# Kernel tuning notes

Measured on AMD Instinct MI355X. Metric: run time of the kernel, lower is better.

Reference implementation:

```python
import jax, jax.numpy as jnp
import numpy as np

NUM_NODES = 100000
NUM_EDGES = 50000
N_INC = 1000000  # incidence pairs (node, hyperedge)
IN_DIM = 128
EDGE_DIM = 128
NODE_DIM = 128


def _glorot(key, fan_in, fan_out):
    lim = float(np.sqrt(6.0 / (fan_in + fan_out)))
    return jax.random.uniform(key, (fan_in, fan_out), jnp.float32, -lim, lim)


def _prelu(x, a):
    return jnp.where(x >= 0, x, a * x)


def setup_inputs() -> dict:
    key = jax.random.key(0)
    ks = jax.random.split(key, 7)
    x = jax.random.normal(ks[0], (NUM_NODES, IN_DIM), jnp.float32)
    node_idx = jax.random.randint(ks[1], (N_INC,), 0, NUM_NODES, jnp.int32)
    edge_idx = jax.random.randint(ks[2], (N_INC,), 0, NUM_EDGES, jnp.int32)
    hyperedge_index = jnp.stack([node_idx, edge_idx])  # [2, N_INC]
    return dict(
        x=x,
        hyperedge_index=hyperedge_index,
        W_n2e_0=_glorot(ks[3], IN_DIM, EDGE_DIM),
        W_e2n_0=_glorot(ks[4], EDGE_DIM, NODE_DIM),
        bias_0=jnp.zeros((NODE_DIM,), jnp.float32),
        W_n2e_1=_glorot(ks[5], NODE_DIM, EDGE_DIM),
        W_e2n_1=_glorot(ks[6], EDGE_DIM, NODE_DIM),
        bias_1=jnp.zeros((NODE_DIM,), jnp.float32),
        alpha=jnp.float32(0.25),  # shared nn.PReLU() parameter
        num_nodes=NUM_NODES,
        num_edges=NUM_EDGES,
    )


def _conv(x, node_idx, edge_idx, Dn_inv, De_inv, W_n2e, W_e2n, b, alpha,
          num_nodes, num_edges):
    # node -> hyperedge: row-normalized scatter-add (norm = De^{-1} per target edge)
    xe = x @ W_n2e                                              # [N, E_dim]
    msg_e = xe[node_idx] * De_inv[edge_idx][:, None]            # [N_INC, E_dim]
    e = jax.ops.segment_sum(msg_e, edge_idx, num_segments=num_edges)
    e = _prelu(e, alpha)
    # hyperedge -> node: norm = Dn^{-1} per target node
    xn = e @ W_e2n                                              # [M, D]
    msg_n = xn[edge_idx] * Dn_inv[node_idx][:, None]            # [N_INC, D]
    n = jax.ops.segment_sum(msg_n, node_idx, num_segments=num_nodes) + b
    return n, e


def reference(x, hyperedge_index, W_n2e_0, W_e2n_0, bias_0, W_n2e_1, W_e2n_1,
              bias_1, alpha, num_nodes, num_edges):
    node_idx = hyperedge_index[0]
    edge_idx = hyperedge_index[1]
    ones = jnp.ones((node_idx.shape[0],), jnp.float32)
    Dn = jax.ops.segment_sum(ones, node_idx, num_segments=num_nodes)
    De = jax.ops.segment_sum(ones, edge_idx, num_segments=num_edges)
    Dn_inv = jnp.where(Dn > 0, 1.0 / jnp.where(Dn > 0, Dn, 1.0), 0.0)
    De_inv = jnp.where(De > 0, 1.0 / jnp.where(De > 0, De, 1.0), 0.0)

    n, e = _conv(x, node_idx, edge_idx, Dn_inv, De_inv,
                 W_n2e_0, W_e2n_0, bias_0, alpha, num_nodes, num_edges)
    n = _prelu(n, alpha)  # encoder-level activation between layers
    n, e = _conv(n, node_idx, edge_idx, Dn_inv, De_inv,
                 W_n2e_1, W_e2n_1, bias_1, alpha, num_nodes, num_edges)
    n = _prelu(n, alpha)
    return n, e
```

## Files before the change

### kernel.cpp

```cpp
#include <hip/hip_runtime.h>
#include <stdint.h>

#define NN 100000
#define NE 50000
#define NBLK 256
#define NBK 196
#define ESH 8
#define NSH 9

using bf16x8 = __attribute__((ext_vector_type(8))) short;
using f32x4  = __attribute__((ext_vector_type(4))) float;

__device__ inline unsigned f2bf(float f) {
  union { float f; unsigned u; } x; x.f = f;
  unsigned u = x.u;
  return (u + 0x7FFFu + ((u >> 16) & 1u)) >> 16;
}
__device__ inline float bfbits2f(unsigned bits) {
  union { unsigned u; float f; } x; x.u = bits;
  return x.f;
}


__global__ __launch_bounds__(256) void hist_kernel(const int* __restrict__ nidx,
                                                   const int* __restrict__ eidx, int ni,
                                                   int* __restrict__ He, int* __restrict__ Hn) {
  __shared__ int he[NBK], hn[NBK];
  for (int t = threadIdx.x; t < NBK; t += 256) { he[t] = 0; hn[t] = 0; }
  __syncthreads();
  int chunk = (ni + NBLK - 1) / NBLK;
  int s = blockIdx.x * chunk, e = min(s + chunk, ni);
  for (int i = s + threadIdx.x; i < e; i += 256) {
    atomicAdd(&he[eidx[i] >> ESH], 1);
    atomicAdd(&hn[nidx[i] >> NSH], 1);
  }
  __syncthreads();
  for (int t = threadIdx.x; t < NBK; t += 256) {
    He[t * NBLK + blockIdx.x] = he[t];
    Hn[t * NBLK + blockIdx.x] = hn[t];
  }
}

__global__ __launch_bounds__(256) void scanH_kernel(int* __restrict__ He, int* __restrict__ Hn,
                                                    int* __restrict__ ebb, int* __restrict__ nbb,
                                                    int ni) {
  int* H = blockIdx.x ? Hn : He;
  int* bb = blockIdx.x ? nbb : ebb;
  __shared__ int tot[256];
  int t = threadIdx.x;
  int sum = 0;
  if (t < NBK)
    for (int b = 0; b < NBLK; b++) sum += H[t * NBLK + b];
  tot[t] = sum;
  __syncthreads();
  for (int o = 1; o < 256; o <<= 1) {
    int v = (t >= o) ? tot[t - o] : 0;
    __syncthreads();
    tot[t] += v;
    __syncthreads();
  }
  int base = (t > 0) ? tot[t - 1] : 0;
  if (t < NBK) {
    bb[t] = base;
    int run = base;
    for (int b = 0; b < NBLK; b++) {
      int old = H[t * NBLK + b];
      H[t * NBLK + b] = run;
      run += old;
    }
  }
  if (t == 0) bb[NBK] = ni;
}

__global__ __launch_bounds__(256) void scatter_kernel(const int* __restrict__ nidx,
                                                      const int* __restrict__ eidx, int ni,
                                                      const int* __restrict__ He,
                                                      const int* __restrict__ Hn,
                                                      int2* __restrict__ binE,
                                                      int2* __restrict__ binN) {
  __shared__ int ce[NBK], cn[NBK];
  for (int t = threadIdx.x; t < NBK; t += 256) {
    ce[t] = He[t * NBLK + blockIdx.x];
    cn[t] = Hn[t * NBLK + blockIdx.x];
  }
  __syncthreads();
  int chunk = (ni + NBLK - 1) / NBLK;
  int s = blockIdx.x * chunk, e = min(s + chunk, ni);
  for (int i = s + threadIdx.x; i < e; i += 256) {
    int nd = nidx[i], ed = eidx[i];
    int pe = atomicAdd(&ce[ed >> ESH], 1);
    binE[pe] = make_int2(nd, ed);
    int pn = atomicAdd(&cn[nd >> NSH], 1);
    binN[pn] = make_int2(ed, nd);
  }
}

__global__ __launch_bounds__(256) void finalize_kernel(const int2* __restrict__ binE,
                                                       const int2* __restrict__ binN,
                                                       const int* __restrict__ ebb,
                                                       const int* __restrict__ nbb,
                                                       int* __restrict__ eoff, int* __restrict__ noff,
                                                       float* __restrict__ einv, float* __restrict__ ninv,
                                                       int* __restrict__ edge_nodes,
                                                       int* __restrict__ node_edges, int ni) {
  __shared__ int cnt[512], excl[512], sc[256];
  bool isE = blockIdx.x < NBK;
  int b = isE ? blockIdx.x : blockIdx.x - NBK;
  const int2* bin = isE ? binE : binN;
  const int* bb = isE ? ebb : nbb;
  int* off = isE ? eoff : noff;
  float* inv = isE ? einv : ninv;
  int* out = isE ? edge_nodes : node_edges;
  int NT = isE ? NE : NN;
  int sh = isE ? ESH : NSH;
  int tbase = b << sh;
  int nt = min(1 << sh, NT - tbase);
  int t = threadIdx.x;
  cnt[t] = 0; cnt[t + 256] = 0;
  __syncthreads();
  int s = bb[b], e = bb[b + 1];
  for (int i = s + t; i < e; i += 256) atomicAdd(&cnt[bin[i].y - tbase], 1);
  __syncthreads();
  int p = cnt[2 * t] + cnt[2 * t + 1];
  sc[t] = p;
  __syncthreads();
  for (int o = 1; o < 256; o <<= 1) {
    int v = (t >= o) ? sc[t - o] : 0;
    __syncthreads();
    sc[t] += v;
    __syncthreads();
  }
  int pb = (t > 0) ? sc[t - 1] : 0;
  excl[2 * t] = pb;
  excl[2 * t + 1] = pb + cnt[2 * t];
  __syncthreads();
  for (int lt = t; lt < nt; lt += 256) {
    off[tbase + lt] = s + excl[lt];
    int c = cnt[lt];
    inv[tbase + lt] = (c > 0) ? 1.0f / (float)c : 0.0f;
  }
  if (b == NBK - 1 && t == 0) off[NT] = ni;
  __syncthreads();
  cnt[t] = 0; cnt[t + 256] = 0;
  __syncthreads();
  for (int i = s + t; i < e; i += 256) {
    int2 it = bin[i];
    int lt = it.y - tbase;
    int pos = s + excl[lt] + atomicAdd(&cnt[lt], 1);
    out[pos] = it.x;
  }
}

__global__ void packw_kernel(const float* __restrict__ w0, const float* __restrict__ w1,
                             const float* __restrict__ w2, const float* __restrict__ w3,
                             short* __restrict__ wp) {
  int gid = blockIdx.x * blockDim.x + threadIdx.x;
  if (gid >= 4 * 16384) return;
  int w = gid >> 14, r = gid & 16383;
  int j = r & 7, lane = (r >> 3) & 63, kk = (r >> 9) & 3, ct = (r >> 11) & 7;
  int k = kk * 32 + (lane >> 4) * 8 + j;
  int c = ct * 16 + (lane & 15);
  const float* W = (w == 0) ? w0 : (w == 1) ? w1 : (w == 2) ? w2 : w3;
  wp[gid] = (short)f2bf(W[k * 128 + c]);
}

template <bool ABF>
__global__ __launch_bounds__(256) void gemm_kernel(const void* __restrict__ Ap,
                                                   const short* __restrict__ Wp,
                                                   short* __restrict__ C, int M) {
  int wave = threadIdx.x >> 6;
  int lane = threadIdx.x & 63;
  int rt = blockIdx.x * 4 + wave;
  if (rt * 16 >= M) return;
  int kg = lane >> 4;
  int rloc = lane & 15;
  bf16x8 a[4];
  if constexpr (ABF) {
    const short* arow = (const short*)Ap + (size_t)(rt * 16 + rloc) * 128 + kg * 8;
#pragma unroll
    for (int kk = 0; kk < 4; kk++) a[kk] = *(const bf16x8*)(arow + kk * 32);
  } else {
    const float* arow = (const float*)Ap + (size_t)(rt * 16 + rloc) * 128 + kg * 8;
#pragma unroll
    for (int kk = 0; kk < 4; kk++) {
      float4 lo = *(const float4*)(arow + kk * 32);
      float4 hi = *(const float4*)(arow + kk * 32 + 4);
      bf16x8 tv;
      tv[0] = (short)f2bf(lo.x); tv[1] = (short)f2bf(lo.y);
      tv[2] = (short)f2bf(lo.z); tv[3] = (short)f2bf(lo.w);
      tv[4] = (short)f2bf(hi.x); tv[5] = (short)f2bf(hi.y);
      tv[6] = (short)f2bf(hi.z); tv[7] = (short)f2bf(hi.w);
      a[kk] = tv;
    }
  }
#pragma unroll
  for (int ct = 0; ct < 8; ct++) {
    f32x4 acc = {0.f, 0.f, 0.f, 0.f};
#pragma unroll
    for (int kk = 0; kk < 4; kk++) {
      bf16x8 bfr = *(const bf16x8*)(Wp + ((size_t)(ct * 4 + kk) * 64 + lane) * 8);
      acc = __builtin_amdgcn_mfma_f32_16x16x32_bf16(a[kk], bfr, acc, 0, 0, 0);
    }
    size_t cbase = (size_t)(rt * 16 + kg * 4) * 128 + ct * 16 + rloc;
#pragma unroll
    for (int j = 0; j < 4; j++) C[cbase + (size_t)j * 128] = (short)f2bf(acc[j]);
  }
}

template <bool OBF>
__global__ __launch_bounds__(256) void gather_kernel(const uint4* __restrict__ src,
                                                     void* __restrict__ dst,
                                                     const int* __restrict__ off,
                                                     const int* __restrict__ ids,
                                                     const float* __restrict__ inv,
                                                     const float* __restrict__ bias,
                                                     const float* __restrict__ alpha_p, int T) {
  int tgt = blockIdx.x * 16 + (threadIdx.x >> 4);
  if (tgt >= T) return;
  int c = threadIdx.x & 15;
  int s = off[tgt], e = off[tgt + 1];
  float a0 = 0, a1 = 0, a2 = 0, a3 = 0, a4 = 0, a5 = 0, a6 = 0, a7 = 0;
  for (int i = s; i < e; i++) {
    int sid = ids[i];
    uint4 v = src[(size_t)sid * 16 + c];
    a0 += bfbits2f(v.x << 16); a1 += bfbits2f(v.x & 0xffff0000u);
    a2 += bfbits2f(v.y << 16); a3 += bfbits2f(v.y & 0xffff0000u);
    a4 += bfbits2f(v.z << 16); a5 += bfbits2f(v.z & 0xffff0000u);
    a6 += bfbits2f(v.w << 16); a7 += bfbits2f(v.w & 0xffff0000u);
  }
  float scv = inv[tgt];
  float al = *alpha_p;
  float b[8] = {0, 0, 0, 0, 0, 0, 0, 0};
  if (bias) {
    float4 b0 = ((const float4*)bias)[c * 2];
    float4 b1 = ((const float4*)bias)[c * 2 + 1];
    b[0] = b0.x; b[1] = b0.y; b[2] = b0.z; b[3] = b0.w;
    b[4] = b1.x; b[5] = b1.y; b[6] = b1.z; b[7] = b1.w;
  }
  float r[8] = {a0, a1, a2, a3, a4, a5, a6, a7};
#pragma unroll
  for (int j = 0; j < 8; j++) {
    float v = r[j] * scv + b[j];
    r[j] = (v >= 0.f) ? v : al * v;
  }
  if constexpr (OBF) {
    uint4 o;
    o.x = (f2bf(r[0]) & 0xffffu) | (f2bf(r[1]) << 16);
    o.y = (f2bf(r[2]) & 0xffffu) | (f2bf(r[3]) << 16);
    o.z = (f2bf(r[4]) & 0xffffu) | (f2bf(r[5]) << 16);
    o.w = (f2bf(r[6]) & 0xffffu) | (f2bf(r[7]) << 16);
    ((uint4*)dst)[(size_t)tgt * 16 + c] = o;
  } else {
    float4 o0; o0.x = r[0]; o0.y = r[1]; o0.z = r[2]; o0.w = r[3];
    float4 o1; o1.x = r[4]; o1.y = r[5]; o1.z = r[6]; o1.w = r[7];
    ((float4*)dst)[(size_t)tgt * 32 + c * 2] = o0;
    ((float4*)dst)[(size_t)tgt * 32 + c * 2 + 1] = o1;
  }
}

extern "C" void kernel_launch(void* const* d_in, const int* in_sizes, int n_in,
                              void* d_out, int out_size, void* d_ws, size_t ws_size,
                              hipStream_t stream) {
  const float* x = (const float*)d_in[0];
  const int* nidx = (const int*)d_in[1];
  int NI = in_sizes[1] / 2;
  const int* eidx = nidx + NI;
  const float* W0 = (const float*)d_in[2];
  const float* W1 = (const float*)d_in[3];
  const float* b0 = (const float*)d_in[4];
  const float* W2 = (const float*)d_in[5];
  const float* W3 = (const float*)d_in[6];
  const float* b1 = (const float*)d_in[7];
  const float* alpha = (const float*)d_in[8];

  char* ws = (char*)d_ws;
  size_t o = 0;
  auto alloc = [&](size_t bytes) { void* p = ws + o; o += (bytes + 255) & ~255ull; return p; };
  int* He = (int*)alloc((size_t)NBK * NBLK * 4);
  int* Hn = (int*)alloc((size_t)NBK * NBLK * 4);
  int* ebb = (int*)alloc((NBK + 1) * 4);
  int* nbb = (int*)alloc((NBK + 1) * 4);
  int* eoff = (int*)alloc((size_t)(NE + 1) * 4);
  int* noff = (int*)alloc((size_t)(NN + 1) * 4);
  float* einv = (float*)alloc((size_t)NE * 4);
  float* ninv = (float*)alloc((size_t)NN * 4);
  int* edge_nodes = (int*)alloc((size_t)NI * 4);
  int* node_edges = (int*)alloc((size_t)NI * 4);
  short* wp = (short*)alloc((size_t)4 * 16384 * 2);
  char* arena = (char*)alloc((size_t)NN * 128 * 2 * 2 + (size_t)NE * 128 * 2 * 2);
  int2* binE = (int2*)arena;
  int2* binN = (int2*)(arena + (size_t)NI * 8);
  short* bufNb = (short*)arena;
  short* bufEb = (short*)(arena + (size_t)NN * 128 * 2);
  short* n0b = (short*)(arena + (size_t)NN * 128 * 2 + (size_t)NE * 128 * 2);
  short* e0b = (short*)(arena + (size_t)NN * 128 * 4 + (size_t)NE * 128 * 2);

  float* outN = (float*)d_out;
  float* outE = outN + (size_t)NN * 128;

  hist_kernel<<<NBLK, 256, 0, stream>>>(nidx, eidx, NI, He, Hn);
  scanH_kernel<<<2, 256, 0, stream>>>(He, Hn, ebb, nbb, NI);
  scatter_kernel<<<NBLK, 256, 0, stream>>>(nidx, eidx, NI, He, Hn, binE, binN);
  finalize_kernel<<<2 * NBK, 256, 0, stream>>>(binE, binN, ebb, nbb, eoff, noff,
                                               einv, ninv, edge_nodes, node_edges, NI);
  packw_kernel<<<256, 256, 0, stream>>>(W0, W1, W2, W3, wp);

  int gN = (NN / 16 + 3) / 4, gE = (NE / 16 + 3) / 4;
  gemm_kernel<false><<<gN, 256, 0, stream>>>(x, wp + 0 * 16384, bufNb, NN);
  gather_kernel<true><<<(NE + 15) / 16, 256, 0, stream>>>((const uint4*)bufNb, e0b,
                                                          eoff, edge_nodes, einv, nullptr, alpha, NE);
  gemm_kernel<true><<<gE, 256, 0, stream>>>(e0b, wp + 1 * 16384, bufEb, NE);
  gather_kernel<true><<<(NN + 15) / 16, 256, 0, stream>>>((const uint4*)bufEb, n0b,
                                                          noff, node_edges, ninv, b0, alpha, NN);
  gemm_kernel<true><<<gN, 256, 0, stream>>>(n0b, wp + 2 * 16384, bufNb, NN);
  gather_kernel<false><<<(NE + 15) / 16, 256, 0, stream>>>((const uint4*)bufNb, outE,
                                                           eoff, edge_nodes, einv, nullptr, alpha, NE);
  gemm_kernel<false><<<gE, 256, 0, stream>>>(outE, wp + 3 * 16384, bufEb, NE);
  gather_kernel<true><<<1, 1, 0, stream>>>((const uint4*)bufEb, e0b, eoff, edge_nodes,
                                           einv, nullptr, alpha, 0);
  gather_kernel<false><<<(NN + 15) / 16, 256, 0, stream>>>((const uint4*)bufEb, outN,
                                                           noff, node_edges, ninv, b1, alpha, NN);
}
```

Measured before the change: 321.0 us.

## Aggregate before projecting and gather from column-chunked bf16 layouts

Uses linearity to swap gather and GEMM in the node-to-edge step: node features are first aggregated per hyperedge, then multiplied by W_n2e. The GEMM therefore runs on 50k edge rows instead of 100k node rows, and the PReLU moves into the GEMM epilogue. Inputs are converted once to bf16 in a column-chunked layout (8 chunks of 16 features, row-major within each chunk). Gather blocks are assigned per chunk so each block touches a smaller source footprint, improving cache locality. The change adds a conversion kernel and a dual fp32/bf16 output, and the rounding order differs slightly from the reference.

```diff
diff --git a/kernel.cpp b/kernel.cpp
--- a/kernel.cpp
+++ b/kernel.cpp
@@ -164,35 +164,63 @@
   wp[gid] = (short)f2bf(W[k * 128 + c]);
 }
 
-template <bool ABF>
+__global__ __launch_bounds__(256) void cvt_kernel(const float* __restrict__ x,
+                                                  uint4* __restrict__ xb) {
+  __shared__ unsigned lds[128 * 65];
+  int t = threadIdx.x;
+  int rows0 = blockIdx.x * 128;
+#pragma unroll
+  for (int it = 0; it < 16; it++) {
+    int q = t + it * 256;
+    int row = q >> 5, f4 = q & 31;
+    if (rows0 + row < NN) {
+      float4 v = ((const float4*)x)[(size_t)(rows0 + row) * 32 + f4];
+      lds[row * 65 + f4 * 2]     = (f2bf(v.x) & 0xffffu) | (f2bf(v.y) << 16);
+      lds[row * 65 + f4 * 2 + 1] = (f2bf(v.z) & 0xffffu) | (f2bf(v.w) << 16);
+    }
+  }
+  __syncthreads();
+#pragma unroll
+  for (int it = 0; it < 8; it++) {
+    int q = t + it * 256;
+    int c = q >> 8, rem = q & 255, row = rem >> 1, h = rem & 1;
+    if (rows0 + row < NN) {
+      unsigned* p = &lds[row * 65 + c * 8 + h * 4];
+      uint4 o; o.x = p[0]; o.y = p[1]; o.z = p[2]; o.w = p[3];
+      xb[((size_t)c * NN + rows0 + row) * 2 + h] = o;
+    }
+  }
+}
+
+template <bool ACHUNK, bool PRELU, int OMODE>
 __global__ __launch_bounds__(256) void gemm_kernel(const void* __restrict__ Ap,
                                                    const short* __restrict__ Wp,
-                                                   short* __restrict__ C, int M) {
+                                                   short* __restrict__ Cb,
+                                                   float* __restrict__ Cf,
+                                                   const float* __restrict__ alpha_p, int M) {
   int wave = threadIdx.x >> 6;
   int lane = threadIdx.x & 63;
   int rt = blockIdx.x * 4 + wave;
   if (rt * 16 >= M) return;
   int kg = lane >> 4;
   int rloc = lane & 15;
+  int row = rt * 16 + rloc;
   bf16x8 a[4];
-  if constexpr (ABF) {
-    const short* arow = (const short*)Ap + (size_t)(rt * 16 + rloc) * 128 + kg * 8;
+  if constexpr (ACHUNK) {
+    const uint4* A = (const uint4*)Ap;
+#pragma unroll
+    for (int kk = 0; kk < 4; kk++) {
+      int c = kk * 2 + (kg >> 1);
+      uint4 v = A[((size_t)c * M + row) * 2 + (kg & 1)];
+      union { uint4 u; bf16x8 b; } cv; cv.u = v;
+      a[kk] = cv.b;
+    }
+  } else {
+    const short* arow = (const short*)Ap + (size_t)row * 128 + kg * 8;
 #pragma unroll
     for (int kk = 0; kk < 4; kk++) a[kk] = *(const bf16x8*)(arow + kk * 32);
-  } else {
-    const float* arow = (const float*)Ap + (size_t)(rt * 16 + rloc) * 128 + kg * 8;
-#pragma unroll
-    for (int kk = 0; kk < 4; kk++) {
-      float4 lo = *(const float4*)(arow + kk * 32);
-      float4 hi = *(const float4*)(arow + kk * 32 + 4);
-      bf16x8 tv;
-      tv[0] = (short)f2bf(lo.x); tv[1] = (short)f2bf(lo.y);
-      tv[2] = (short)f2bf(lo.z); tv[3] = (short)f2bf(lo.w);
-      tv[4] = (short)f2bf(hi.x); tv[5] = (short)f2bf(hi.y);
-      tv[6] = (short)f2bf(hi.z); tv[7] = (short)f2bf(hi.w);
-      a[kk] = tv;
-    }
-  }
+  }
+  float al = PRELU ? *alpha_p : 0.f;
 #pragma unroll
   for (int ct = 0; ct < 8; ct++) {
     f32x4 acc = {0.f, 0.f, 0.f, 0.f};
@@ -201,60 +229,77 @@
       bf16x8 bfr = *(const bf16x8*)(Wp + ((size_t)(ct * 4 + kk) * 64 + lane) * 8);
       acc = __builtin_amdgcn_mfma_f32_16x16x32_bf16(a[kk], bfr, acc, 0, 0, 0);
     }
-    size_t cbase = (size_t)(rt * 16 + kg * 4) * 128 + ct * 16 + rloc;
-#pragma unroll
-    for (int j = 0; j < 4; j++) C[cbase + (size_t)j * 128] = (short)f2bf(acc[j]);
-  }
-}
-
-template <bool OBF>
-__global__ __launch_bounds__(256) void gather_kernel(const uint4* __restrict__ src,
-                                                     void* __restrict__ dst,
-                                                     const int* __restrict__ off,
-                                                     const int* __restrict__ ids,
-                                                     const float* __restrict__ inv,
-                                                     const float* __restrict__ bias,
-                                                     const float* __restrict__ alpha_p, int T) {
-  int tgt = blockIdx.x * 16 + (threadIdx.x >> 4);
+    int col = ct * 16 + rloc;
+#pragma unroll
+    for (int j = 0; j < 4; j++) {
+      int rj = rt * 16 + kg * 4 + j;
+      float v = acc[j];
+      if constexpr (PRELU) v = (v >= 0.f) ? v : al * v;
+      if constexpr (OMODE == 0) {
+        Cb[(size_t)rj * 128 + col] = (short)f2bf(v);
+      } else if constexpr (OMODE == 1) {
+        Cb[((size_t)ct * M + rj) * 16 + rloc] = (short)f2bf(v);
+      } else {
+        Cf[(size_t)rj * 128 + col] = v;
+        Cb[(size_t)rj * 128 + col] = (short)f2bf(v);
+      }
+    }
+  }
+}
+
+template <bool PRELU, int OUT>
+__global__ __launch_bounds__(256) void gatherc_kernel(const uint4* __restrict__ src,
+                                                      void* __restrict__ dst,
+                                                      const int* __restrict__ off,
+                                                      const int* __restrict__ ids,
+                                                      const float* __restrict__ inv,
+                                                      const float* __restrict__ bias,
+                                                      const float* __restrict__ alpha_p,
+                                                      int T, int Rsrc) {
+  int c = blockIdx.x & 7;
+  int grp = blockIdx.x >> 3;
+  int p = threadIdx.x >> 1, h = threadIdx.x & 1;
+  int tgt = grp * 128 + p;
   if (tgt >= T) return;
-  int c = threadIdx.x & 15;
   int s = off[tgt], e = off[tgt + 1];
-  float a0 = 0, a1 = 0, a2 = 0, a3 = 0, a4 = 0, a5 = 0, a6 = 0, a7 = 0;
+  const uint4* base = src + (size_t)c * Rsrc * 2 + h;
+  float r0 = 0, r1 = 0, r2 = 0, r3 = 0, r4 = 0, r5 = 0, r6 = 0, r7 = 0;
   for (int i = s; i < e; i++) {
-    int sid = ids[i];
-    uint4 v = src[(size_t)sid * 16 + c];
-    a0 += bfbits2f(v.x << 16); a1 += bfbits2f(v.x & 0xffff0000u);
-    a2 += bfbits2f(v.y << 16); a3 += bfbits2f(v.y & 0xffff0000u);
-    a4 += bfbits2f(v.z << 16); a5 += bfbits2f(v.z & 0xffff0000u);
-    a6 += bfbits2f(v.w << 16); a7 += bfbits2f(v.w & 0xffff0000u);
+    int id = ids[i];
+    uint4 v = base[(size_t)id * 2];
+    r0 += bfbits2f(v.x << 16); r1 += bfbits2f(v.x & 0xffff0000u);
+    r2 += bfbits2f(v.y << 16); r3 += bfbits2f(v.y & 0xffff0000u);
+    r4 += bfbits2f(v.z << 16); r5 += bfbits2f(v.z & 0xffff0000u);
+    r6 += bfbits2f(v.w << 16); r7 += bfbits2f(v.w & 0xffff0000u);
   }
   float scv = inv[tgt];
-  float al = *alpha_p;
+  float r[8] = {r0, r1, r2, r3, r4, r5, r6, r7};
   float b[8] = {0, 0, 0, 0, 0, 0, 0, 0};
   if (bias) {
-    float4 b0 = ((const float4*)bias)[c * 2];
-    float4 b1 = ((const float4*)bias)[c * 2 + 1];
+    float4 b0 = ((const float4*)bias)[c * 4 + h * 2];
+    float4 b1 = ((const float4*)bias)[c * 4 + h * 2 + 1];
     b[0] = b0.x; b[1] = b0.y; b[2] = b0.z; b[3] = b0.w;
     b[4] = b1.x; b[5] = b1.y; b[6] = b1.z; b[7] = b1.w;
   }
-  float r[8] = {a0, a1, a2, a3, a4, a5, a6, a7};
+  float al = PRELU ? *alpha_p : 0.f;
 #pragma unroll
   for (int j = 0; j < 8; j++) {
     float v = r[j] * scv + b[j];
-    r[j] = (v >= 0.f) ? v : al * v;
-  }
-  if constexpr (OBF) {
+    if constexpr (PRELU) v = (v >= 0.f) ? v : al * v;
+    r[j] = v;
+  }
+  if constexpr (OUT == 0) {
     uint4 o;
     o.x = (f2bf(r[0]) & 0xffffu) | (f2bf(r[1]) << 16);
     o.y = (f2bf(r[2]) & 0xffffu) | (f2bf(r[3]) << 16);
     o.z = (f2bf(r[4]) & 0xffffu) | (f2bf(r[5]) << 16);
     o.w = (f2bf(r[6]) & 0xffffu) | (f2bf(r[7]) << 16);
-    ((uint4*)dst)[(size_t)tgt * 16 + c] = o;
+    ((uint4*)dst)[((size_t)c * T + tgt) * 2 + h] = o;
   } else {
     float4 o0; o0.x = r[0]; o0.y = r[1]; o0.z = r[2]; o0.w = r[3];
     float4 o1; o1.x = r[4]; o1.y = r[5]; o1.z = r[6]; o1.w = r[7];
-    ((float4*)dst)[(size_t)tgt * 32 + c * 2] = o0;
-    ((float4*)dst)[(size_t)tgt * 32 + c * 2 + 1] = o1;
+    ((float4*)dst)[(size_t)tgt * 32 + c * 4 + h * 2] = o0;
+    ((float4*)dst)[(size_t)tgt * 32 + c * 4 + h * 2 + 1] = o1;
   }
 }
 
@@ -287,13 +332,13 @@
   int* edge_nodes = (int*)alloc((size_t)NI * 4);
   int* node_edges = (int*)alloc((size_t)NI * 4);
   short* wp = (short*)alloc((size_t)4 * 16384 * 2);
-  char* arena = (char*)alloc((size_t)NN * 128 * 2 * 2 + (size_t)NE * 128 * 2 * 2);
+  char* arena = (char*)alloc((size_t)NN * 128 * 2 + (size_t)NE * 128 * 2 * 3);
   int2* binE = (int2*)arena;
   int2* binN = (int2*)(arena + (size_t)NI * 8);
-  short* bufNb = (short*)arena;
-  short* bufEb = (short*)(arena + (size_t)NN * 128 * 2);
-  short* n0b = (short*)(arena + (size_t)NN * 128 * 2 + (size_t)NE * 128 * 2);
-  short* e0b = (short*)(arena + (size_t)NN * 128 * 4 + (size_t)NE * 128 * 2);
+  uint4* xb  = (uint4*)arena;
+  uint4* Geb = (uint4*)(arena + (size_t)NN * 128 * 2);
+  short* eb  = (short*)(arena + (size_t)NN * 128 * 2 + (size_t)NE * 128 * 2);
+  short* xnb = (short*)(arena + (size_t)NN * 128 * 2 + (size_t)NE * 128 * 2 * 2);
 
   float* outN = (float*)d_out;
   float* outE = outN + (size_t)NN * 128;
@@ -304,20 +349,23 @@
   finalize_kernel<<<2 * NBK, 256, 0, stream>>>(binE, binN, ebb, nbb, eoff, noff,
                                                einv, ninv, edge_nodes, node_edges, NI);
   packw_kernel<<<256, 256, 0, stream>>>(W0, W1, W2, W3, wp);
-
-  int gN = (NN / 16 + 3) / 4, gE = (NE / 16 + 3) / 4;
-  gemm_kernel<false><<<gN, 256, 0, stream>>>(x, wp + 0 * 16384, bufNb, NN);
-  gather_kernel<true><<<(NE + 15) / 16, 256, 0, stream>>>((const uint4*)bufNb, e0b,
-                                                          eoff, edge_nodes, einv, nullptr, alpha, NE);
-  gemm_kernel<true><<<gE, 256, 0, stream>>>(e0b, wp + 1 * 16384, bufEb, NE);
-  gather_kernel<true><<<(NN + 15) / 16, 256, 0, stream>>>((const uint4*)bufEb, n0b,
-                                                          noff, node_edges, ninv, b0, alpha, NN);
-  gemm_kernel<true><<<gN, 256, 0, stream>>>(n0b, wp + 2 * 16384, bufNb, NN);
-  gather_kernel<false><<<(NE + 15) / 16, 256, 0, stream>>>((const uint4*)bufNb, outE,
-                                                           eoff, edge_nodes, einv, nullptr, alpha, NE);
-  gemm_kernel<false><<<gE, 256, 0, stream>>>(outE, wp + 3 * 16384, bufEb, NE);
-  gather_kernel<true><<<1, 1, 0, stream>>>((const uint4*)bufEb, e0b, eoff, edge_nodes,
-                                           einv, nullptr, alpha, 0);
-  gather_kernel<false><<<(NN + 15) / 16, 256, 0, stream>>>((const uint4*)bufEb, outN,
-                                                           noff, node_edges, ninv, b1, alpha, NN);
-}
+  cvt_kernel<<<(NN + 127) / 128, 256, 0, stream>>>(x, xb);
+
+  int gE = ((NE / 16) + 3) / 4;
+  int ggE = ((NE + 127) / 128) * 8;
+  int ggN = ((NN + 127) / 128) * 8;
+
+  gatherc_kernel<false, 0><<<ggE, 256, 0, stream>>>(xb, Geb, eoff, edge_nodes,
+                                                    einv, nullptr, alpha, NE, NN);
+  gemm_kernel<true, true, 0><<<gE, 256, 0, stream>>>(Geb, wp + 0 * 16384, eb, nullptr, alpha, NE);
+  gemm_kernel<false, false, 1><<<gE, 256, 0, stream>>>(eb, wp + 1 * 16384, xnb, nullptr, alpha, NE);
+  uint4* n1b = xb;
+  gatherc_kernel<true, 0><<<ggN, 256, 0, stream>>>((const uint4*)xnb, n1b, noff, node_edges,
+                                                   ninv, b0, alpha, NN, NE);
+  gatherc_kernel<false, 0><<<ggE, 256, 0, stream>>>(n1b, Geb, eoff, edge_nodes,
+                                                    einv, nullptr, alpha, NE, NN);
+  gemm_kernel<true, true, 2><<<gE, 256, 0, stream>>>(Geb, wp + 2 * 16384, eb, outE, alpha, NE);
+  gemm_kernel<false, false, 1><<<gE, 256, 0, stream>>>(eb, wp + 3 * 16384, xnb, nullptr, alpha, NE);
+  gatherc_kernel<true, 1><<<ggN, 256, 0, stream>>>((const uint4*)xnb, outN, noff, node_edges,
+                                                   ninv, b1, alpha, NN, NE);
+}
```

After: 485.0 us. 1.51x slower.

## Aggregate before transform so node-to-edge GEMMs run on edge rows

Applied to the files above, without the earlier changes.

Uses linearity of the scatter-mean to gather raw node features into hyperedges first and apply W_n2e afterwards. The n2e GEMMs then run over 50k edge rows instead of 100k node rows, and PReLU is fused into the GEMM epilogue. It also adds a standalone fp32-to-bf16 conversion of x and unrolls the gather loop by 8 to keep more independent loads in flight. The trade-off is that rounding changes because aggregation now happens before the matmul in bf16, and the x conversion adds an extra pass.

```diff
diff --git a/kernel.cpp b/kernel.cpp
--- a/kernel.cpp
+++ b/kernel.cpp
@@ -164,35 +164,37 @@
   wp[gid] = (short)f2bf(W[k * 128 + c]);
 }
 
-template <bool ABF>
-__global__ __launch_bounds__(256) void gemm_kernel(const void* __restrict__ Ap,
+__global__ __launch_bounds__(256) void cvtrow_kernel(const float* __restrict__ x,
+                                                     uint4* __restrict__ xb) {
+  size_t q = (size_t)blockIdx.x * 256 + threadIdx.x;
+  const float4* xf = (const float4*)x;
+  float4 lo = xf[q * 2], hi = xf[q * 2 + 1];
+  uint4 o;
+  o.x = (f2bf(lo.x) & 0xffffu) | (f2bf(lo.y) << 16);
+  o.y = (f2bf(lo.z) & 0xffffu) | (f2bf(lo.w) << 16);
+  o.z = (f2bf(hi.x) & 0xffffu) | (f2bf(hi.y) << 16);
+  o.w = (f2bf(hi.z) & 0xffffu) | (f2bf(hi.w) << 16);
+  xb[q] = o;
+}
+
+template <bool PRELU, int OMODE>
+__global__ __launch_bounds__(256) void gemm_kernel(const short* __restrict__ Ap,
                                                    const short* __restrict__ Wp,
-                                                   short* __restrict__ C, int M) {
+                                                   short* __restrict__ Cb,
+                                                   float* __restrict__ Cf,
+                                                   const float* __restrict__ alpha_p, int M) {
   int wave = threadIdx.x >> 6;
   int lane = threadIdx.x & 63;
   int rt = blockIdx.x * 4 + wave;
   if (rt * 16 >= M) return;
   int kg = lane >> 4;
   int rloc = lane & 15;
+  int row = rt * 16 + rloc;
+  const short* arow = Ap + (size_t)row * 128 + kg * 8;
   bf16x8 a[4];
-  if constexpr (ABF) {
-    const short* arow = (const short*)Ap + (size_t)(rt * 16 + rloc) * 128 + kg * 8;
-#pragma unroll
-    for (int kk = 0; kk < 4; kk++) a[kk] = *(const bf16x8*)(arow + kk * 32);
-  } else {
-    const float* arow = (const float*)Ap + (size_t)(rt * 16 + rloc) * 128 + kg * 8;
-#pragma unroll
-    for (int kk = 0; kk < 4; kk++) {
-      float4 lo = *(const float4*)(arow + kk * 32);
-      float4 hi = *(const float4*)(arow + kk * 32 + 4);
-      bf16x8 tv;
-      tv[0] = (short)f2bf(lo.x); tv[1] = (short)f2bf(lo.y);
-      tv[2] = (short)f2bf(lo.z); tv[3] = (short)f2bf(lo.w);
-      tv[4] = (short)f2bf(hi.x); tv[5] = (short)f2bf(hi.y);
-      tv[6] = (short)f2bf(hi.z); tv[7] = (short)f2bf(hi.w);
-      a[kk] = tv;
-    }
-  }
+#pragma unroll
+  for (int kk = 0; kk < 4; kk++) a[kk] = *(const bf16x8*)(arow + kk * 32);
+  float al = PRELU ? *alpha_p : 0.f;
 #pragma unroll
   for (int ct = 0; ct < 8; ct++) {
     f32x4 acc = {0.f, 0.f, 0.f, 0.f};
@@ -201,13 +203,23 @@
       bf16x8 bfr = *(const bf16x8*)(Wp + ((size_t)(ct * 4 + kk) * 64 + lane) * 8);
       acc = __builtin_amdgcn_mfma_f32_16x16x32_bf16(a[kk], bfr, acc, 0, 0, 0);
     }
-    size_t cbase = (size_t)(rt * 16 + kg * 4) * 128 + ct * 16 + rloc;
-#pragma unroll
-    for (int j = 0; j < 4; j++) C[cbase + (size_t)j * 128] = (short)f2bf(acc[j]);
-  }
-}
-
-template <bool OBF>
+    int col = ct * 16 + rloc;
+#pragma unroll
+    for (int j = 0; j < 4; j++) {
+      int rj = rt * 16 + kg * 4 + j;
+      float v = acc[j];
+      if constexpr (PRELU) v = (v >= 0.f) ? v : al * v;
+      if constexpr (OMODE == 0) {
+        Cb[(size_t)rj * 128 + col] = (short)f2bf(v);
+      } else {
+        Cf[(size_t)rj * 128 + col] = v;
+        Cb[(size_t)rj * 128 + col] = (short)f2bf(v);
+      }
+    }
+  }
+}
+
+template <bool PRELU, bool OBF>
 __global__ __launch_bounds__(256) void gather_kernel(const uint4* __restrict__ src,
                                                      void* __restrict__ dst,
                                                      const int* __restrict__ off,
@@ -219,17 +231,32 @@
   if (tgt >= T) return;
   int c = threadIdx.x & 15;
   int s = off[tgt], e = off[tgt + 1];
-  float a0 = 0, a1 = 0, a2 = 0, a3 = 0, a4 = 0, a5 = 0, a6 = 0, a7 = 0;
-  for (int i = s; i < e; i++) {
-    int sid = ids[i];
-    uint4 v = src[(size_t)sid * 16 + c];
-    a0 += bfbits2f(v.x << 16); a1 += bfbits2f(v.x & 0xffff0000u);
-    a2 += bfbits2f(v.y << 16); a3 += bfbits2f(v.y & 0xffff0000u);
-    a4 += bfbits2f(v.z << 16); a5 += bfbits2f(v.z & 0xffff0000u);
-    a6 += bfbits2f(v.w << 16); a7 += bfbits2f(v.w & 0xffff0000u);
+  float r[8] = {0, 0, 0, 0, 0, 0, 0, 0};
+  int i = s;
+  for (; i + 8 <= e; i += 8) {
+    int idv[8];
+#pragma unroll
+    for (int u = 0; u < 8; u++) idv[u] = ids[i + u];
+    uint4 v[8];
+#pragma unroll
+    for (int u = 0; u < 8; u++) v[u] = src[(size_t)idv[u] * 16 + c];
+#pragma unroll
+    for (int u = 0; u < 8; u++) {
+      r[0] += bfbits2f(v[u].x << 16); r[1] += bfbits2f(v[u].x & 0xffff0000u);
+      r[2] += bfbits2f(v[u].y << 16); r[3] += bfbits2f(v[u].y & 0xffff0000u);
+      r[4] += bfbits2f(v[u].z << 16); r[5] += bfbits2f(v[u].z & 0xffff0000u);
+      r[6] += bfbits2f(v[u].w << 16); r[7] += bfbits2f(v[u].w & 0xffff0000u);
+    }
+  }
+  for (; i < e; i++) {
+    uint4 v = src[(size_t)ids[i] * 16 + c];
+    r[0] += bfbits2f(v.x << 16); r[1] += bfbits2f(v.x & 0xffff0000u);
+    r[2] += bfbits2f(v.y << 16); r[3] += bfbits2f(v.y & 0xffff0000u);
+    r[4] += bfbits2f(v.z << 16); r[5] += bfbits2f(v.z & 0xffff0000u);
+    r[6] += bfbits2f(v.w << 16); r[7] += bfbits2f(v.w & 0xffff0000u);
   }
   float scv = inv[tgt];
-  float al = *alpha_p;
+  float al = PRELU ? *alpha_p : 0.f;
   float b[8] = {0, 0, 0, 0, 0, 0, 0, 0};
   if (bias) {
     float4 b0 = ((const float4*)bias)[c * 2];
@@ -237,11 +264,11 @@
     b[0] = b0.x; b[1] = b0.y; b[2] = b0.z; b[3] = b0.w;
     b[4] = b1.x; b[5] = b1.y; b[6] = b1.z; b[7] = b1.w;
   }
-  float r[8] = {a0, a1, a2, a3, a4, a5, a6, a7};
 #pragma unroll
   for (int j = 0; j < 8; j++) {
     float v = r[j] * scv + b[j];
-    r[j] = (v >= 0.f) ? v : al * v;
+    if constexpr (PRELU) v = (v >= 0.f) ? v : al * v;
+    r[j] = v;
   }
   if constexpr (OBF) {
     uint4 o;
@@ -287,13 +314,13 @@
   int* edge_nodes = (int*)alloc((size_t)NI * 4);
   int* node_edges = (int*)alloc((size_t)NI * 4);
   short* wp = (short*)alloc((size_t)4 * 16384 * 2);
-  char* arena = (char*)alloc((size_t)NN * 128 * 2 * 2 + (size_t)NE * 128 * 2 * 2);
+  char* arena = (char*)alloc((size_t)NN * 128 * 2 + (size_t)NE * 128 * 2 * 3);
   int2* binE = (int2*)arena;
   int2* binN = (int2*)(arena + (size_t)NI * 8);
-  short* bufNb = (short*)arena;
-  short* bufEb = (short*)(arena + (size_t)NN * 128 * 2);
-  short* n0b = (short*)(arena + (size_t)NN * 128 * 2 + (size_t)NE * 128 * 2);
-  short* e0b = (short*)(arena + (size_t)NN * 128 * 4 + (size_t)NE * 128 * 2);
+  short* xb = (short*)arena;
+  short* Ge = (short*)(arena + (size_t)NN * 128 * 2);
+  short* eb = (short*)(arena + (size_t)NN * 128 * 2 + (size_t)NE * 128 * 2);
+  short* xn = (short*)(arena + (size_t)NN * 128 * 2 + (size_t)NE * 128 * 2 * 2);
 
   float* outN = (float*)d_out;
   float* outE = outN + (size_t)NN * 128;
@@ -304,20 +331,23 @@
   finalize_kernel<<<2 * NBK, 256, 0, stream>>>(binE, binN, ebb, nbb, eoff, noff,
                                                einv, ninv, edge_nodes, node_edges, NI);
   packw_kernel<<<256, 256, 0, stream>>>(W0, W1, W2, W3, wp);
-
-  int gN = (NN / 16 + 3) / 4, gE = (NE / 16 + 3) / 4;
-  gemm_kernel<false><<<gN, 256, 0, stream>>>(x, wp + 0 * 16384, bufNb, NN);
-  gather_kernel<true><<<(NE + 15) / 16, 256, 0, stream>>>((const uint4*)bufNb, e0b,
-                                                          eoff, edge_nodes, einv, nullptr, alpha, NE);
-  gemm_kernel<true><<<gE, 256, 0, stream>>>(e0b, wp + 1 * 16384, bufEb, NE);
-  gather_kernel<true><<<(NN + 15) / 16, 256, 0, stream>>>((const uint4*)bufEb, n0b,
-                                                          noff, node_edges, ninv, b0, alpha, NN);
-  gemm_kernel<true><<<gN, 256, 0, stream>>>(n0b, wp + 2 * 16384, bufNb, NN);
-  gather_kernel<false><<<(NE + 15) / 16, 256, 0, stream>>>((const uint4*)bufNb, outE,
-                                                           eoff, edge_nodes, einv, nullptr, alpha, NE);
-  gemm_kernel<false><<<gE, 256, 0, stream>>>(outE, wp + 3 * 16384, bufEb, NE);
-  gather_kernel<true><<<1, 1, 0, stream>>>((const uint4*)bufEb, e0b, eoff, edge_nodes,
-                                           einv, nullptr, alpha, 0);
-  gather_kernel<false><<<(NN + 15) / 16, 256, 0, stream>>>((const uint4*)bufEb, outN,
-                                                           noff, node_edges, ninv, b1, alpha, NN);
-}
+  cvtrow_kernel<<<NN * 128 / 8 / 256, 256, 0, stream>>>(x, (uint4*)xb);
+
+  int gE = ((NE / 16) + 3) / 4;
+  int ggE = NE / 16;
+  int ggN = (NN + 15) / 16;
+
+  gather_kernel<false, true><<<ggE, 256, 0, stream>>>((const uint4*)xb, Ge, eoff, edge_nodes,
+                                                      einv, nullptr, alpha, NE);
+  gemm_kernel<true, 0><<<gE, 256, 0, stream>>>(Ge, wp + 0 * 16384, eb, nullptr, alpha, NE);
+  gemm_kernel<false, 0><<<gE, 256, 0, stream>>>(eb, wp + 1 * 16384, xn, nullptr, alpha, NE);
+  short* n1 = xb;
+  gather_kernel<true, true><<<ggN, 256, 0, stream>>>((const uint4*)xn, n1, noff, node_edges,
+                                                     ninv, b0, alpha, NN);
+  gather_kernel<false, true><<<ggE, 256, 0, stream>>>((const uint4*)n1, Ge, eoff, edge_nodes,
+                                                      einv, nullptr, alpha, NE);
+  gemm_kernel<true, 2><<<gE, 256, 0, stream>>>(Ge, wp + 2 * 16384, eb, outE, alpha, NE);
+  gemm_kernel<false, 0><<<gE, 256, 0, stream>>>(eb, wp + 3 * 16384, xn, nullptr, alpha, NE);
+  gather_kernel<true, false><<<ggN, 256, 0, stream>>>((const uint4*)xn, outN, noff, node_edges,
+                                                      ninv, b1, alpha, NN);
+}
```

New measurement: 299.4 us. 1.07x faster.
